# Performance work log

Measured on AMD Instinct MI355X. Metric: run time of the kernel, lower is better.

## Reference

```python
import jax, jax.numpy as jnp
import numpy as np

B, S, HID = 2, 2048, 1024
H, D = 16, 64  # num query heads, head_dim; single shared KV head
SCALE = D ** -0.5


def setup_inputs() -> dict:
    key = jax.random.key(0)
    k1, k2, k3, k4, k5 = jax.random.split(key, 5)
    return {
        "hidden_states": jax.random.normal(k1, (B, S, HID), dtype=jnp.float32),
        "Wq": jax.random.normal(k2, (HID, HID), dtype=jnp.float32) * 0.02,
        "Wk": jax.random.normal(k3, (HID, D), dtype=jnp.float32) * 0.02,
        "Wv": jax.random.normal(k4, (HID, D), dtype=jnp.float32) * 0.02,
        "Wo": jax.random.normal(k5, (HID, HID), dtype=jnp.float32) * 0.02,
    }


def reference(hidden_states, Wq, Wk, Wv, Wo):
    b, s, _ = hidden_states.shape
    # projections: Q has H heads; K/V have a single shared head of dim D
    q = (hidden_states @ Wq).reshape(b, s, H, D)  # [B,S,H,D]
    k = hidden_states @ Wk                        # [B,S,D]
    v = hidden_states @ Wv                        # [B,S,D]
    # scores: broadcast single KV head across all query heads
    scores = jnp.einsum("bqhd,bkd->bhqk", q, k) * SCALE  # [B,H,S,S]
    attn = jax.nn.softmax(scores, axis=-1)
    out = jnp.einsum("bhqk,bkd->bqhd", attn, v).reshape(b, s, HID)
    return out @ Wo
```

## Files before the change

### kernel.cpp

```cpp
#include <hip/hip_runtime.h>
#include <math.h>

#define BATCH 2
#define SEQ   2048
#define HID   1024
#define NH    16
#define HD    64
#define MTOT  (BATCH * SEQ)

#define PST 72
#define VST 136
#define WTS 69
#define FBUF 35840
#define KTS  9216
#define VTS  8704

#define EXP_C1 0.1803368801111255f

typedef __attribute__((ext_vector_type(8))) short short8;
typedef __attribute__((ext_vector_type(4))) float floatx4;
typedef __attribute__((ext_vector_type(16))) float floatx16;
typedef __attribute__((ext_vector_type(4))) unsigned int uint4v;

#define MFMA32(a, b, c) __builtin_amdgcn_mfma_f32_32x32x16_bf16(a, b, c, 0, 0, 0)
#define MFMA16(a, b, c) __builtin_amdgcn_mfma_f32_16x16x32_bf16(a, b, c, 0, 0, 0)

static __device__ __forceinline__ floatx16 zero16() {
    floatx16 z;
    #pragma unroll
    for (int i = 0; i < 16; ++i) z[i] = 0.f;
    return z;
}

__device__ __forceinline__ unsigned short f2bf(float x) {
    unsigned u = __float_as_uint(x);
    u += 0x7FFF + ((u >> 16) & 1);
    return (unsigned short)(u >> 16);
}
__device__ __forceinline__ float bf2f(unsigned short h) {
    return __uint_as_float((unsigned)h << 16);
}

__device__ __forceinline__ void gld16(const unsigned short* g, unsigned short* l) {
    __builtin_amdgcn_global_load_lds(
        (const __attribute__((address_space(1))) unsigned int*)g,
        (__attribute__((address_space(3))) unsigned int*)l, 16, 0, 0);
}

__device__ __forceinline__ unsigned packtr(unsigned hi, unsigned lo) {
    return __builtin_amdgcn_perm(hi, lo, 0x07060302u);
}


__global__ __launch_bounds__(256)
void presplit_kernel(const float* __restrict__ Wq, const float* __restrict__ Wk,
                     const float* __restrict__ Wv, const float* __restrict__ Wo,
                     const float* __restrict__ X,
                     unsigned short* __restrict__ WqTh,
                     unsigned short* __restrict__ WkTh,
                     unsigned short* __restrict__ WvTh,
                     unsigned short* __restrict__ WoTh, unsigned short* __restrict__ WoTl,
                     unsigned short* __restrict__ Xh)
{
    __shared__ __align__(16) float Wtmp[64][WTS];
    const int tid = threadIdx.x;
    int bx = blockIdx.x;

    if (bx >= 544) {
        size_t i0 = (size_t)(bx - 544) * 4096 + tid * 16;
        float f[16];
        *(float4*)&f[0]  = *(const float4*)(X + i0 + 0);
        *(float4*)&f[4]  = *(const float4*)(X + i0 + 4);
        *(float4*)&f[8]  = *(const float4*)(X + i0 + 8);
        *(float4*)&f[12] = *(const float4*)(X + i0 + 12);
        unsigned short hh[16];
        #pragma unroll
        for (int e = 0; e < 16; ++e) hh[e] = f2bf(f[e]);
        const int m  = (bx - 544) * 4 + (tid >> 6);
        const int k0 = (tid & 63) * 16;
        const int m32 = m >> 5, mi = (m >> 4) & 1, tr = m & 15;
        #pragma unroll
        for (int c = 0; c < 2; ++c) {
            const int k = k0 + c * 8;
            const int ktx = k >> 6, ksx = (k >> 5) & 1, qd = (k >> 3) & 3;
            size_t off = (((size_t)(m32 * 16 + ktx) * 2 + ksx) * 2 + mi) * 512
                       + (qd * 16 + tr) * 8;
            *(uint4*)(Xh + off) = *(uint4*)&hh[c * 8];
        }
        return;
    }

    const float* W; unsigned short *Th, *Tl; int ldw, kt, nt;
    if (bx < 256)      { W = Wq; Th = WqTh; Tl = nullptr; ldw = HID; kt = bx >> 4; nt = bx & 15; }
    else if (bx < 272) { W = Wk; Th = WkTh; Tl = nullptr; ldw = HD;  kt = bx - 256; nt = 0; }
    else if (bx < 288) { W = Wv; Th = WvTh; Tl = nullptr; ldw = HD;  kt = bx - 272; nt = 0; }
    else               { W = Wo; Th = WoTh; Tl = WoTl;   ldw = HID; bx -= 288; kt = bx >> 4; nt = bx & 15; }
    const int k0 = kt * 64, n0 = nt * 64;

    {
        const int wk = tid >> 2, wn = (tid & 3) * 16;
        const float* wp = W + (size_t)(k0 + wk) * ldw + n0 + wn;
        float f[16];
        *(float4*)&f[0]  = *(const float4*)(wp + 0);
        *(float4*)&f[4]  = *(const float4*)(wp + 4);
        *(float4*)&f[8]  = *(const float4*)(wp + 8);
        *(float4*)&f[12] = *(const float4*)(wp + 12);
        #pragma unroll
        for (int e = 0; e < 16; ++e) Wtmp[wk][wn + e] = f[e];
    }
    __syncthreads();
    {
        const int rn = tid >> 2, rk = (tid & 3) * 16;
        float f[16];
        #pragma unroll
        for (int e = 0; e < 16; ++e) f[e] = Wtmp[rk + e][rn];
        unsigned short hh[16];
        #pragma unroll
        for (int e = 0; e < 16; ++e) hh[e] = f2bf(f[e]);
        const int sub = rn >> 4, tw = rn & 15;
        const size_t tb = ((size_t)nt * 16 + kt) * 4096;
        const int ksA = rk >> 5,       qA = (rk >> 3) & 3;
        const int ksB = (rk + 8) >> 5, qB = ((rk + 8) >> 3) & 3;
        const size_t offA = tb + (size_t)(ksA * 4 + sub) * 512 + (qA * 16 + tw) * 8;
        const size_t offB = tb + (size_t)(ksB * 4 + sub) * 512 + (qB * 16 + tw) * 8;
        *(uint4*)(Th + offA) = *(uint4*)&hh[0];
        *(uint4*)(Th + offB) = *(uint4*)&hh[8];
        if (Tl) {
            unsigned short ll[16];
            #pragma unroll
            for (int e = 0; e < 16; ++e) ll[e] = f2bf(f[e] - bf2f(hh[e]));
            *(uint4*)(Tl + offA) = *(uint4*)&ll[0];
            *(uint4*)(Tl + offB) = *(uint4*)&ll[8];
        }
    }
}

__global__ __launch_bounds__(512)
void qkv_kernel(const unsigned short* __restrict__ Xfo,
                const unsigned short* __restrict__ WqTh,
                const unsigned short* __restrict__ WkTh,
                const unsigned short* __restrict__ WvTh,
                unsigned short* __restrict__ Qh,
                unsigned short* __restrict__ Khf, unsigned short* __restrict__ Vthf)
{
    __shared__ __align__(16) unsigned short Wst[2][4096];

    const int tid  = threadIdx.x;
    const int wave = tid >> 6, lane = tid & 63;
    const int t = lane & 15, quad = lane >> 4;
    const int m0 = blockIdx.x * 128;
    const int nb = blockIdx.y;

    const unsigned short *WTh; int nt;
    if (nb < 16)       { WTh = WqTh; nt = nb; }
    else if (nb == 16) { WTh = WkTh; nt = 0; }
    else               { WTh = WvTh; nt = 0; }

    floatx4 acc[4];
    #pragma unroll
    for (int sub = 0; sub < 4; ++sub) acc[sub] = (floatx4){0.f,0.f,0.f,0.f};

    const int m32 = blockIdx.x * 4 + (wave >> 1), mi = wave & 1;
    const size_t abase = ((size_t)m32 * 16) * 2048 + (size_t)mi * 512 + lane * 8;

    auto STAGE = [&](int buf, int kt) {
        const size_t tb = ((size_t)nt * 16 + kt) * 4096 + wave * 512 + lane * 8;
        gld16(WTh + tb, &Wst[buf][wave * 512]);
    };
    auto COMPUTE = [&](int buf, short8 a0, short8 a1) {
        #pragma unroll
        for (int ksq = 0; ksq < 2; ++ksq) {
            short8 am = ksq ? a1 : a0;
            #pragma unroll
            for (int sub = 0; sub < 4; ++sub) {
                short8 bh = *(const short8*)&Wst[buf][(ksq * 4 + sub) * 512 + lane * 8];
                acc[sub] = MFMA16(am, bh, acc[sub]);
            }
        }
    };

    short8 a0 = *(const short8*)(Xfo + abase);
    short8 a1 = *(const short8*)(Xfo + abase + 1024);
    STAGE(0, 0);
    __syncthreads();

    int cur = 0;
    for (int kt = 0; kt < HID / 64 - 1; ++kt) {
        STAGE(cur ^ 1, kt + 1);
        short8 n0 = *(const short8*)(Xfo + abase + (size_t)(kt + 1) * 2048);
        short8 n1 = *(const short8*)(Xfo + abase + (size_t)(kt + 1) * 2048 + 1024);

        COMPUTE(cur, a0, a1);

        __syncthreads();
        a0 = n0; a1 = n1;
        cur ^= 1;
    }
    COMPUTE(cur, a0, a1);

    #pragma unroll
    for (int sub = 0; sub < 4; ++sub)
        #pragma unroll
        for (int r = 0; r < 4; ++r) {
            int g = m0 + wave * 16 + quad * 4 + r;
            int d = sub * 16 + t;
            if (nb < 16) {
                int b = g >> 11, s = g & (SEQ - 1);
                Qh[((size_t)(b * NH + nb) * SEQ + s) * HD + d] =
                    f2bf(acc[sub][r] * EXP_C1);
            } else if (nb == 16) {
                int b = g >> 11, s = g & (SEQ - 1);
                int tt = s >> 7, sl = s & 127;
                Khf[(size_t)(b * 16 + tt) * KTS + sl * PST + d] = f2bf(acc[sub][r]);
            } else {
                int b = g >> 11, s = g & (SEQ - 1);
                int tt = s >> 7, sl = s & 127;
                Vthf[(size_t)(b * 16 + tt) * VTS + d * VST + sl] = f2bf(acc[sub][r]);
            }
        }
}

__global__ __launch_bounds__(512, 4)
void flash_kernel(const unsigned short* __restrict__ Qhg,
                  const unsigned short* __restrict__ Khf,
                  const unsigned short* __restrict__ Vthf,
                  unsigned short* __restrict__ Oh)
{
    extern __shared__ __align__(16) char smem[];

    const int tid  = threadIdx.x;
    const int wave = tid >> 6, lane = tid & 63;
    const int lq = lane & 31, hi = lane >> 5;
    const int qw = wave >> 1;
    const int ks = wave & 1;
    const int klq = (lq & ~12) | ((lq & 4) << 1) | ((lq & 8) >> 1);

    const int q0 = blockIdx.x * 128;
    const int h  = blockIdx.y;
    const int b  = blockIdx.z;

    short8 qreg[4];
    {
        const unsigned short* qp =
            Qhg + ((size_t)(b * NH + h) * SEQ + q0 + qw * 32 + lq) * HD + hi * 8;
        #pragma unroll
        for (int dc = 0; dc < 4; ++dc) qreg[dc] = *(const short8*)(qp + dc * 16);
    }

    const unsigned short* Kb = Khf  + (size_t)b * 16 * KTS;
    const unsigned short* Vb = Vthf + (size_t)b * 16 * VTS;

    floatx16 o0 = zero16(), o1 = zero16(), ol = zero16();
    short8 onesB;
    #pragma unroll
    for (int j = 0; j < 8; ++j) onesB[j] = (short)0x3F80;

    const int NT = SEQ / 128;

    auto STAGE = [&](int buf, int kt2) {
        const unsigned short* KG = Kb + (size_t)kt2 * KTS;
        const unsigned short* VG = Vb + (size_t)kt2 * VTS;
        unsigned short* Kl = (unsigned short*)(smem + buf * FBUF);
        unsigned short* Vl = (unsigned short*)(smem + buf * FBUF + 18432);
        gld16(KG + (size_t)tid * 8,          Kl + wave * 512);
        gld16(KG + (size_t)(512 + tid) * 8,  Kl + (512 + wave * 64) * 8);
        gld16(VG + (size_t)tid * 8,          Vl + wave * 512);
        gld16(VG + (size_t)(512 + tid) * 8,  Vl + (512 + wave * 64) * 8);
        if (tid < 128) gld16(KG + (size_t)(1024 + tid) * 8, Kl + (1024 + wave * 64) * 8);
        if (tid < 64)  gld16(VG + (size_t)(1024 + tid) * 8, Vl + (1024 + wave * 64) * 8);
    };

    STAGE(0, 0);
    __syncthreads();

    for (int kt = 0; kt < NT; ++kt) {
        char* base = smem + (kt & 1) * FBUF;
        unsigned short (*Ksh)[PST] = (unsigned short (*)[PST])base;
        unsigned short (*Vsh)[VST] = (unsigned short (*)[VST])(base + 18432);

        if (kt + 1 < NT) STAGE((kt + 1) & 1, kt + 1);

        const int kb0 = ks * 64, kb1 = ks * 64 + 32;
        floatx16 sfA = zero16(), sfB = zero16();
        __builtin_amdgcn_s_setprio(1);
        #pragma unroll
        for (int dc = 0; dc < 4; ++dc) {
            short8 kfA = *(const short8*)&Ksh[kb0 + klq][dc * 16 + hi * 8];
            sfA = MFMA32(kfA, qreg[dc], sfA);
        }
        #pragma unroll
        for (int dc = 0; dc < 4; ++dc) {
            short8 kfB = *(const short8*)&Ksh[kb1 + klq][dc * 16 + hi * 8];
            sfB = MFMA32(kfB, qreg[dc], sfB);
        }
        __builtin_amdgcn_s_setprio(0);

        auto PROCESS = [&](const floatx16& sf, int kb) {
            #pragma unroll
            for (int mm = 0; mm < 2; ++mm) {
                unsigned uu[8];
                #pragma unroll
                for (int j = 0; j < 8; ++j)
                    uu[j] = __float_as_uint(exp2f(sf[mm * 8 + j]));
                uint4v pw;
                pw.x = packtr(uu[1], uu[0]);
                pw.y = packtr(uu[3], uu[2]);
                pw.z = packtr(uu[5], uu[4]);
                pw.w = packtr(uu[7], uu[6]);
                short8 pa = __builtin_bit_cast(short8, pw);
                short8 v0 = *(const short8*)&Vsh[lq][kb + mm * 16 + hi * 8];
                short8 v1 = *(const short8*)&Vsh[32 + lq][kb + mm * 16 + hi * 8];
                __builtin_amdgcn_s_setprio(1);
                ol = MFMA32(pa, onesB, ol);
                o0 = MFMA32(pa, v0, o0);
                o1 = MFMA32(pa, v1, o1);
                __builtin_amdgcn_s_setprio(0);
            }
        };

        PROCESS(sfA, kb0);
        PROCESS(sfB, kb1);
        __syncthreads();
    }

    float* cb  = (float*)smem;
    float* cbl = (float*)(smem + 33792);
    const int cbase = (qw * 64 + lane) * 33;
    if (ks) {
        #pragma unroll
        for (int r = 0; r < 16; ++r) { cb[cbase + r] = o0[r]; cb[cbase + 16 + r] = o1[r]; }
        if (lq == 0) {
            #pragma unroll
            for (int r = 0; r < 16; ++r) cbl[(qw * 2 + hi) * 16 + r] = ol[r];
        }
    }
    __syncthreads();
    if (!ks) {
        const int m32 = b * 64 + blockIdx.x * 4 + qw;
        #pragma unroll
        for (int r = 0; r < 16; ++r) {
            int qr = (r & 3) + 8 * (r >> 2) + 4 * hi;
            float ltot = ol[r] + cbl[(qw * 2 + hi) * 16 + r];
            float inv = 1.0f / ltot;
            float a0 = o0[r] + cb[cbase + r];
            float a1 = o1[r] + cb[cbase + 16 + r];
            int mi = qr >> 4, tr = qr & 15;
            size_t base = (((size_t)(m32 * 16 + h) * 2 + 0) * 2 + mi) * 512
                        + ((lq >> 3) * 16 + tr) * 8 + (lq & 7);
            Oh[base]        = f2bf(a0 * inv);
            Oh[base + 1024] = f2bf(a1 * inv);
        }
    }
}

__global__ __launch_bounds__(512)
void out_proj_kernel(const unsigned short* __restrict__ Ofo,
                     const unsigned short* __restrict__ WoTh,
                     const unsigned short* __restrict__ WoTl,
                     float* __restrict__ out)
{
    __shared__ __align__(16) unsigned short Wst[2][2][4096];

    const int tid  = threadIdx.x;
    const int wave = tid >> 6, lane = tid & 63;
    const int t = lane & 15, quad = lane >> 4;
    const int m0 = blockIdx.x * 128;
    const int nt = blockIdx.y;

    floatx4 acc[4];
    #pragma unroll
    for (int sub = 0; sub < 4; ++sub) acc[sub] = (floatx4){0.f,0.f,0.f,0.f};

    const int m32 = blockIdx.x * 4 + (wave >> 1), mi = wave & 1;
    const size_t abase = ((size_t)m32 * 16) * 2048 + (size_t)mi * 512 + lane * 8;

    auto STAGE = [&](int buf, int kt) {
        const size_t tb = ((size_t)nt * 16 + kt) * 4096 + wave * 512 + lane * 8;
        gld16(WoTh + tb, &Wst[buf][0][wave * 512]);
        gld16(WoTl + tb, &Wst[buf][1][wave * 512]);
    };
    auto COMPUTE = [&](int buf, short8 a0, short8 a1) {
        #pragma unroll
        for (int ksq = 0; ksq < 2; ++ksq) {
            short8 am = ksq ? a1 : a0;
            #pragma unroll
            for (int sub = 0; sub < 4; ++sub) {
                short8 bh = *(const short8*)&Wst[buf][0][(ksq * 4 + sub) * 512 + lane * 8];
                short8 bl = *(const short8*)&Wst[buf][1][(ksq * 4 + sub) * 512 + lane * 8];
                acc[sub] = MFMA16(am, bh, acc[sub]);
                acc[sub] = MFMA16(am, bl, acc[sub]);
            }
        }
    };

    short8 a0 = *(const short8*)(Ofo + abase);
    short8 a1 = *(const short8*)(Ofo + abase + 1024);
    STAGE(0, 0);
    __syncthreads();

    int cur = 0;
    for (int kt = 0; kt < HID / 64 - 1; ++kt) {
        STAGE(cur ^ 1, kt + 1);
        short8 n0 = *(const short8*)(Ofo + abase + (size_t)(kt + 1) * 2048);
        short8 n1 = *(const short8*)(Ofo + abase + (size_t)(kt + 1) * 2048 + 1024);

        COMPUTE(cur, a0, a1);

        __syncthreads();
        a0 = n0; a1 = n1;
        cur ^= 1;
    }
    COMPUTE(cur, a0, a1);

    const int n0 = nt * 64;
    #pragma unroll
    for (int sub = 0; sub < 4; ++sub)
        #pragma unroll
        for (int r = 0; r < 4; ++r)
            out[(size_t)(m0 + wave * 16 + quad * 4 + r) * HID
                + n0 + sub * 16 + t] = acc[sub][r];
}

extern "C" void kernel_launch(void* const* d_in, const int* in_sizes, int n_in,
                              void* d_out, int out_size, void* d_ws, size_t ws_size,
                              hipStream_t stream)
{
    const float* X  = (const float*)d_in[0];
    const float* Wq = (const float*)d_in[1];
    const float* Wk = (const float*)d_in[2];
    const float* Wv = (const float*)d_in[3];
    const float* Wo = (const float*)d_in[4];
    float* out = (float*)d_out;

    unsigned short* Qh = (unsigned short*)d_out;
    unsigned short* Xh = Qh + (size_t)BATCH * NH * SEQ * HD;

    char* ws = (char*)d_ws;
    const size_t SZ_WQ = (size_t)HID * HID * 2;
    const size_t SZ_WK = (size_t)HD * HID * 2;
    unsigned short* WqTh = (unsigned short*)(ws);
    unsigned short* WkTh = (unsigned short*)(ws + SZ_WQ);
    unsigned short* WvTh = (unsigned short*)(ws + SZ_WQ + SZ_WK);
    unsigned short* WoTh = (unsigned short*)(ws + SZ_WQ + 2*SZ_WK);
    unsigned short* WoTl = (unsigned short*)(ws + 2*SZ_WQ + 2*SZ_WK);
    unsigned short* Khf  = (unsigned short*)(ws + 3*SZ_WQ + 2*SZ_WK);
    unsigned short* Vthf = Khf + (size_t)BATCH * 16 * KTS;
    unsigned short* Oh   = Vthf + (size_t)BATCH * 16 * VTS;

    presplit_kernel<<<dim3(1568), 256, 0, stream>>>(Wq, Wk, Wv, Wo, X,
        WqTh, WkTh, WvTh, WoTh, WoTl, Xh);
    qkv_kernel<<<dim3(MTOT / 128, 18), 512, 0, stream>>>(Xh,
        WqTh, WkTh, WvTh, Qh, Khf, Vthf);
    flash_kernel<<<dim3(SEQ / 128, NH, BATCH), 512, 2 * FBUF, stream>>>(Qh, Khf, Vthf, Oh);
    out_proj_kernel<<<dim3(MTOT / 128, HID / 64), 512, 0, stream>>>(Oh, WoTh, WoTl, out);
}
```

Baseline: 170.2 us.

## Split flash attention into 64-query blocks with per-wave head-dim split

Each flash block now covers 64 queries and steps through 64-key tiles, with waves split across query group, key half and head-dim half. The K/V tile layout changes to match, and shared memory per block is halved. The row-sum is now accumulated on scalar ALUs from bf16-truncated probabilities and combined with shuffles, instead of using an MFMA against a ones vector. This gives twice as many blocks, higher occupancy and fewer MFMAs per block, at the cost of more tile iterations, more barriers and QK^T being recomputed for each head-dim half.

```diff
diff --git a/kernel.cpp b/kernel.cpp
--- a/kernel.cpp
+++ b/kernel.cpp
@@ -9,11 +9,9 @@
 #define MTOT  (BATCH * SEQ)
 
 #define PST 72
-#define VST 136
 #define WTS 69
-#define FBUF 35840
-#define KTS  9216
-#define VTS  8704
+#define KTS 4608
+#define FBUF 18432
 
 #define EXP_C1 0.1803368801111255f
 
@@ -210,17 +208,17 @@
                     f2bf(acc[sub][r] * EXP_C1);
             } else if (nb == 16) {
                 int b = g >> 11, s = g & (SEQ - 1);
-                int tt = s >> 7, sl = s & 127;
-                Khf[(size_t)(b * 16 + tt) * KTS + sl * PST + d] = f2bf(acc[sub][r]);
+                Khf[(size_t)(b * 32 + (s >> 6)) * KTS + (s & 63) * PST + d] =
+                    f2bf(acc[sub][r]);
             } else {
                 int b = g >> 11, s = g & (SEQ - 1);
-                int tt = s >> 7, sl = s & 127;
-                Vthf[(size_t)(b * 16 + tt) * VTS + d * VST + sl] = f2bf(acc[sub][r]);
+                Vthf[(size_t)(b * 32 + (s >> 6)) * KTS + d * PST + (s & 63)] =
+                    f2bf(acc[sub][r]);
             }
         }
 }
 
-__global__ __launch_bounds__(512, 4)
+__global__ __launch_bounds__(512, 8)
 void flash_kernel(const unsigned short* __restrict__ Qhg,
                   const unsigned short* __restrict__ Khf,
                   const unsigned short* __restrict__ Vthf,
@@ -231,11 +229,12 @@
     const int tid  = threadIdx.x;
     const int wave = tid >> 6, lane = tid & 63;
     const int lq = lane & 31, hi = lane >> 5;
-    const int qw = wave >> 1;
-    const int ks = wave & 1;
+    const int qw = wave >> 2;
+    const int ks = (wave >> 1) & 1;
+    const int ds = wave & 1;
     const int klq = (lq & ~12) | ((lq & 4) << 1) | ((lq & 8) >> 1);
 
-    const int q0 = blockIdx.x * 128;
+    const int q0 = blockIdx.x * 64;
     const int h  = blockIdx.y;
     const int b  = blockIdx.z;
 
@@ -247,27 +246,25 @@
         for (int dc = 0; dc < 4; ++dc) qreg[dc] = *(const short8*)(qp + dc * 16);
     }
 
-    const unsigned short* Kb = Khf  + (size_t)b * 16 * KTS;
-    const unsigned short* Vb = Vthf + (size_t)b * 16 * VTS;
-
-    floatx16 o0 = zero16(), o1 = zero16(), ol = zero16();
-    short8 onesB;
-    #pragma unroll
-    for (int j = 0; j < 8; ++j) onesB[j] = (short)0x3F80;
-
-    const int NT = SEQ / 128;
-
-    auto STAGE = [&](int buf, int kt2) {
-        const unsigned short* KG = Kb + (size_t)kt2 * KTS;
-        const unsigned short* VG = Vb + (size_t)kt2 * VTS;
+    const unsigned short* Kb = Khf  + (size_t)b * 32 * KTS;
+    const unsigned short* Vb = Vthf + (size_t)b * 32 * KTS;
+
+    floatx16 o = zero16();
+    float l_part = 0.f;
+
+    const int NT = SEQ / 64;
+
+    auto STAGE = [&](int buf, int t2) {
+        const unsigned short* KG = Kb + (size_t)t2 * KTS;
+        const unsigned short* VG = Vb + (size_t)t2 * KTS;
         unsigned short* Kl = (unsigned short*)(smem + buf * FBUF);
-        unsigned short* Vl = (unsigned short*)(smem + buf * FBUF + 18432);
-        gld16(KG + (size_t)tid * 8,          Kl + wave * 512);
-        gld16(KG + (size_t)(512 + tid) * 8,  Kl + (512 + wave * 64) * 8);
-        gld16(VG + (size_t)tid * 8,          Vl + wave * 512);
-        gld16(VG + (size_t)(512 + tid) * 8,  Vl + (512 + wave * 64) * 8);
-        if (tid < 128) gld16(KG + (size_t)(1024 + tid) * 8, Kl + (1024 + wave * 64) * 8);
-        if (tid < 64)  gld16(VG + (size_t)(1024 + tid) * 8, Vl + (1024 + wave * 64) * 8);
+        unsigned short* Vl = (unsigned short*)(smem + buf * FBUF + 9216);
+        gld16(KG + (size_t)tid * 8, Kl + wave * 512);
+        gld16(VG + (size_t)tid * 8, Vl + wave * 512);
+        if (tid < 64) {
+            gld16(KG + (size_t)(512 + tid) * 8, Kl + 4096);
+            gld16(VG + (size_t)(512 + tid) * 8, Vl + 4096);
+        }
     };
 
     STAGE(0, 0);
@@ -276,79 +273,65 @@
     for (int kt = 0; kt < NT; ++kt) {
         char* base = smem + (kt & 1) * FBUF;
         unsigned short (*Ksh)[PST] = (unsigned short (*)[PST])base;
-        unsigned short (*Vsh)[VST] = (unsigned short (*)[VST])(base + 18432);
+        unsigned short (*Vsh)[PST] = (unsigned short (*)[PST])(base + 9216);
 
         if (kt + 1 < NT) STAGE((kt + 1) & 1, kt + 1);
 
-        const int kb0 = ks * 64, kb1 = ks * 64 + 32;
-        floatx16 sfA = zero16(), sfB = zero16();
+        floatx16 sf = zero16();
         __builtin_amdgcn_s_setprio(1);
         #pragma unroll
         for (int dc = 0; dc < 4; ++dc) {
-            short8 kfA = *(const short8*)&Ksh[kb0 + klq][dc * 16 + hi * 8];
-            sfA = MFMA32(kfA, qreg[dc], sfA);
-        }
-        #pragma unroll
-        for (int dc = 0; dc < 4; ++dc) {
-            short8 kfB = *(const short8*)&Ksh[kb1 + klq][dc * 16 + hi * 8];
-            sfB = MFMA32(kfB, qreg[dc], sfB);
+            short8 kf = *(const short8*)&Ksh[ks * 32 + klq][dc * 16 + hi * 8];
+            sf = MFMA32(kf, qreg[dc], sf);
         }
         __builtin_amdgcn_s_setprio(0);
 
-        auto PROCESS = [&](const floatx16& sf, int kb) {
+        #pragma unroll
+        for (int mm = 0; mm < 2; ++mm) {
+            unsigned uu[8];
             #pragma unroll
-            for (int mm = 0; mm < 2; ++mm) {
-                unsigned uu[8];
-                #pragma unroll
-                for (int j = 0; j < 8; ++j)
-                    uu[j] = __float_as_uint(exp2f(sf[mm * 8 + j]));
-                uint4v pw;
-                pw.x = packtr(uu[1], uu[0]);
-                pw.y = packtr(uu[3], uu[2]);
-                pw.z = packtr(uu[5], uu[4]);
-                pw.w = packtr(uu[7], uu[6]);
-                short8 pa = __builtin_bit_cast(short8, pw);
-                short8 v0 = *(const short8*)&Vsh[lq][kb + mm * 16 + hi * 8];
-                short8 v1 = *(const short8*)&Vsh[32 + lq][kb + mm * 16 + hi * 8];
-                __builtin_amdgcn_s_setprio(1);
-                ol = MFMA32(pa, onesB, ol);
-                o0 = MFMA32(pa, v0, o0);
-                o1 = MFMA32(pa, v1, o1);
-                __builtin_amdgcn_s_setprio(0);
-            }
-        };
-
-        PROCESS(sfA, kb0);
-        PROCESS(sfB, kb1);
+            for (int j = 0; j < 8; ++j)
+                uu[j] = __float_as_uint(exp2f(sf[mm * 8 + j]));
+            #pragma unroll
+            for (int j = 0; j < 8; ++j)
+                l_part += __uint_as_float(uu[j] & 0xFFFF0000u);
+            uint4v pw;
+            pw.x = packtr(uu[1], uu[0]);
+            pw.y = packtr(uu[3], uu[2]);
+            pw.z = packtr(uu[5], uu[4]);
+            pw.w = packtr(uu[7], uu[6]);
+            short8 pa = __builtin_bit_cast(short8, pw);
+            short8 v = *(const short8*)&Vsh[ds * 32 + lq][ks * 32 + mm * 16 + hi * 8];
+            __builtin_amdgcn_s_setprio(1);
+            o = MFMA32(pa, v, o);
+            __builtin_amdgcn_s_setprio(0);
+        }
         __syncthreads();
     }
 
-    float* cb  = (float*)smem;
-    float* cbl = (float*)(smem + 33792);
-    const int cbase = (qw * 64 + lane) * 33;
+    float l_full = l_part + __shfl_xor(l_part, 32);
+    __syncthreads();
+    float* cb = (float*)smem;
+    const int w2 = qw * 2 + ds;
+    const int cbase = (w2 * 64 + lane) * 17;
     if (ks) {
         #pragma unroll
-        for (int r = 0; r < 16; ++r) { cb[cbase + r] = o0[r]; cb[cbase + 16 + r] = o1[r]; }
-        if (lq == 0) {
-            #pragma unroll
-            for (int r = 0; r < 16; ++r) cbl[(qw * 2 + hi) * 16 + r] = ol[r];
-        }
+        for (int r = 0; r < 16; ++r) cb[cbase + r] = o[r];
+        cb[cbase + 16] = l_full;
     }
     __syncthreads();
     if (!ks) {
-        const int m32 = b * 64 + blockIdx.x * 4 + qw;
+        float ltot = l_full + cb[cbase + 16];
+        const int m32 = b * 64 + blockIdx.x * 2 + qw;
         #pragma unroll
         for (int r = 0; r < 16; ++r) {
             int qr = (r & 3) + 8 * (r >> 2) + 4 * hi;
-            float ltot = ol[r] + cbl[(qw * 2 + hi) * 16 + r];
-            float inv = 1.0f / ltot;
-            float a0 = o0[r] + cb[cbase + r];
-            float a1 = o1[r] + cb[cbase + 16 + r];
+            float inv = 1.0f / __shfl(ltot, qr);
+            float a = o[r] + cb[cbase + r];
             int mi = qr >> 4, tr = qr & 15;
             size_t base = (((size_t)(m32 * 16 + h) * 2 + 0) * 2 + mi) * 512
                         + ((lq >> 3) * 16 + tr) * 8 + (lq & 7);
-            Oh[base]        = f2bf(a0 * inv);
-            Oh[base + 1024] = f2bf(a1 * inv);
+            Oh[base + (size_t)ds * 1024] = f2bf(a * inv);
         }
     }
 }
@@ -444,13 +427,13 @@
     unsigned short* WoTh = (unsigned short*)(ws + SZ_WQ + 2*SZ_WK);
     unsigned short* WoTl = (unsigned short*)(ws + 2*SZ_WQ + 2*SZ_WK);
     unsigned short* Khf  = (unsigned short*)(ws + 3*SZ_WQ + 2*SZ_WK);
-    unsigned short* Vthf = Khf + (size_t)BATCH * 16 * KTS;
-    unsigned short* Oh   = Vthf + (size_t)BATCH * 16 * VTS;
+    unsigned short* Vthf = Khf + (size_t)BATCH * 32 * KTS;
+    unsigned short* Oh   = Vthf + (size_t)BATCH * 32 * KTS;
 
     presplit_kernel<<<dim3(1568), 256, 0, stream>>>(Wq, Wk, Wv, Wo, X,
         WqTh, WkTh, WvTh, WoTh, WoTl, Xh);
     qkv_kernel<<<dim3(MTOT / 128, 18), 512, 0, stream>>>(Xh,
         WqTh, WkTh, WvTh, Qh, Khf, Vthf);
-    flash_kernel<<<dim3(SEQ / 128, NH, BATCH), 512, 2 * FBUF, stream>>>(Qh, Khf, Vthf, Oh);
+    flash_kernel<<<dim3(SEQ / 64, NH, BATCH), 512, 2 * FBUF, stream>>>(Qh, Khf, Vthf, Oh);
     out_proj_kernel<<<dim3(MTOT / 128, HID / 64), 512, 0, stream>>>(Oh, WoTh, WoTl, out);
 }
```

New measurement: 236.6 us. 1.39x slower.
